# Kernel optimization log

Hardware: AMD Instinct MI355X
Metric: run time of the kernel (lower is better)

## Reference

```python
import jax, jax.numpy as jnp
import numpy as np

N = 100000
E = 1600000
D_IN = 128
HID = 128
OUT = 64


def _sage_conv(x, edge_index, W_l, W_r, b, num_nodes):
    # PyG SAGEConv (aggr='mean'): out = lin_l(mean_{j in N(i)} x_j) + lin_r(x_i)
    src, dst = edge_index[0], edge_index[1]
    msgs = x[src]  # [E, d] gather from source nodes
    summed = jax.ops.segment_sum(msgs, dst, num_segments=num_nodes)  # [N, d]
    cnt = jax.ops.segment_sum(jnp.ones((msgs.shape[0],), x.dtype), dst, num_segments=num_nodes)
    agg = summed / jnp.maximum(cnt, 1.0)[:, None]  # mean; isolated nodes -> 0
    return agg @ W_l + b + x @ W_r


def setup_inputs() -> dict:
    key = jax.random.key(0)
    ks = jax.random.split(key, 8)
    x = jax.random.normal(ks[0], (N, D_IN), dtype=jnp.float32)
    edge_index = jax.random.randint(ks[1], (2, E), 0, N, dtype=jnp.int64)
    s1 = 1.0 / np.sqrt(D_IN)
    s2 = 1.0 / np.sqrt(HID)
    W_l1 = jax.random.uniform(ks[2], (D_IN, HID), jnp.float32, -s1, s1)
    W_r1 = jax.random.uniform(ks[3], (D_IN, HID), jnp.float32, -s1, s1)
    b1 = jnp.zeros((HID,), jnp.float32)
    W_l2 = jax.random.uniform(ks[4], (HID, OUT), jnp.float32, -s2, s2)
    W_r2 = jax.random.uniform(ks[5], (HID, OUT), jnp.float32, -s2, s2)
    b2 = jnp.zeros((OUT,), jnp.float32)
    return {"x": x, "edge_index": edge_index, "W_l1": W_l1, "W_r1": W_r1,
            "b1": b1, "W_l2": W_l2, "W_r2": W_r2, "b2": b2}


def reference(x, edge_index, W_l1, W_r1, b1, W_l2, W_r2, b2):
    h = _sage_conv(x, edge_index, W_l1, W_r1, b1, N)
    h = jax.nn.relu(h)
    out = _sage_conv(h, edge_index, W_l2, W_r2, b2, N)
    return out
```

## Files before the change

kernel.cpp:

```cpp
#include <hip/hip_runtime.h>
#include <hip/hip_fp16.h>

typedef __attribute__((ext_vector_type(8))) short bf16x8;
typedef __attribute__((ext_vector_type(4))) float f32x4;

__device__ __forceinline__ f32x4 mfma16(bf16x8 a, bf16x8 b, f32x4 c) {
    return __builtin_amdgcn_mfma_f32_16x16x32_bf16(a, b, c, 0, 0, 0);
}

__device__ __forceinline__ unsigned short bf16_rte(float f) {
    unsigned int u = __float_as_uint(f);
    unsigned int r = (u + 0x7FFFu + ((u >> 16) & 1u)) >> 16;
    return (unsigned short)r;
}
__device__ __forceinline__ float bf16_f(unsigned short h) {
    return __uint_as_float(((unsigned int)h) << 16);
}

__global__ void k_wconv(const float* __restrict__ W, unsigned short* __restrict__ hi,
                        unsigned short* __restrict__ lo, int K, int F) {
    int e = blockIdx.x * 256 + threadIdx.x;
    if (e >= K * F) return;
    int col = e / K, k = e - col * K;
    float v = W[(size_t)k * F + col];
    unsigned short h = bf16_rte(v);
    hi[e] = h;
    lo[e] = bf16_rte(v - bf16_f(h));
}


#define MAXNB 1024

__global__ __launch_bounds__(256) void k_bcount(
    const int* __restrict__ dst, int* __restrict__ bcnt, int E, int chunk, int nb) {
    __shared__ int h[MAXNB];
    int t = threadIdx.x;
    for (int i = t; i < nb; i += 256) h[i] = 0;
    __syncthreads();
    int base = blockIdx.x * chunk;
    int end = min(base + chunk, E);
    for (int i = base + t; i < end; i += 256) atomicAdd(&h[dst[i] >> 7], 1);
    __syncthreads();
    for (int i = t; i < nb; i += 256)
        if (h[i]) atomicAdd(&bcnt[i], h[i]);
}

__global__ void k_bscan(const int* __restrict__ bcnt, int* __restrict__ boff,
                        int* __restrict__ bcur, int nb) {
    __shared__ int sh[1024];
    int t = threadIdx.x;
    int v = (t < nb) ? bcnt[t] : 0;
    sh[t] = v;
    __syncthreads();
    for (int off = 1; off < 1024; off <<= 1) {
        int u = (t >= off) ? sh[t - off] : 0;
        __syncthreads();
        sh[t] += u;
        __syncthreads();
    }
    if (t < nb) {
        int ex = sh[t] - v;
        boff[t] = ex;
        bcur[t] = ex;
    }
}

__global__ __launch_bounds__(256) void k_bscatter(
    const int* __restrict__ src, const int* __restrict__ dst,
    int* __restrict__ bcur, int2* __restrict__ pairs, int E, int chunk, int nb) {
    __shared__ int h[MAXNB];
    __shared__ int curs[MAXNB];
    int t = threadIdx.x;
    for (int i = t; i < nb; i += 256) h[i] = 0;
    __syncthreads();
    int base = blockIdx.x * chunk;
    int end = min(base + chunk, E);
    for (int i = base + t; i < end; i += 256) atomicAdd(&h[dst[i] >> 7], 1);
    __syncthreads();
    for (int i = t; i < nb; i += 256)
        curs[i] = h[i] ? atomicAdd(&bcur[i], h[i]) : 0;
    __syncthreads();
    for (int i = base + t; i < end; i += 256) {
        int d = dst[i];
        int p = atomicAdd(&curs[d >> 7], 1);
        pairs[p] = make_int2(d, src[i]);
    }
}

__global__ __launch_bounds__(256) void k_build(
    const int2* __restrict__ pairs, const int* __restrict__ boff,
    int* __restrict__ csr, int* __restrict__ start, int* __restrict__ deg,
    int n, int nb, int E) {
    __shared__ int scnt[128];
    __shared__ int soff[128];
    __shared__ int cur[128];
    int b = blockIdx.x;
    int t = threadIdx.x;
    int base = boff[b];
    int end = (b + 1 < nb) ? boff[b + 1] : E;
    if (t < 128) scnt[t] = 0;
    __syncthreads();
    for (int i = base + t; i < end; i += 256) {
        int2 e = pairs[i];
        atomicAdd(&scnt[e.x & 127], 1);
    }
    __syncthreads();
    if (t < 128) soff[t] = scnt[t];
    __syncthreads();
    for (int off = 1; off < 128; off <<= 1) {
        int val = 0;
        if (t < 128 && t >= off) val = soff[t - off];
        __syncthreads();
        if (t < 128) soff[t] += val;
        __syncthreads();
    }
    if (t < 128) {
        int c = scnt[t];
        int ex = soff[t] - c;
        int node = b * 128 + t;
        if (node < n) {
            start[node] = base + ex;
            deg[node] = c;
        }
        cur[t] = base + ex;
    }
    __syncthreads();
    for (int i = base + t; i < end; i += 256) {
        int2 e = pairs[i];
        int p = atomicAdd(&cur[e.x & 127], 1);
        csr[p] = e.y;
    }
}


#define SR 40

template <int FOUT>
__device__ __forceinline__ void gemm_fused_body(
    const float* __restrict__ X,
    const unsigned short* __restrict__ WHa, const unsigned short* __restrict__ WLa,
    const unsigned short* __restrict__ WHb, const unsigned short* __restrict__ WLb,
    const float* __restrict__ bias, __half* __restrict__ dstH,
    float* __restrict__ dstF, int n) {
    constexpr int CT = FOUT / 32;
    __shared__ unsigned short aHi[64 * SR], aLo[64 * SR];

    int t = threadIdx.x;
    int wv = t >> 6, l = t & 63, q = l >> 4, nl = l & 15;
    int ysel = wv >> 1;
    int wc = (wv & 1) * (FOUT / 2);
    int node0 = blockIdx.x * 64;
    const unsigned short* WH = ysel ? WHb : WHa;
    const unsigned short* WL = ysel ? WLb : WLa;

    int sn = t >> 2, q4 = t & 3;
    int gn = min(node0 + sn, n - 1);
    const float4* ap = (const float4*)(X + (size_t)gn * 128);

    f32x4 acc[4][CT];
#pragma unroll
    for (int a = 0; a < 4; ++a)
#pragma unroll
        for (int b = 0; b < CT; ++b) acc[a][b] = (f32x4){0.f, 0.f, 0.f, 0.f};

    float4 a0 = ap[q4 * 2];
    float4 a1 = ap[q4 * 2 + 1];

    bf16x8 wh[2][CT], wl[2][CT];
#pragma unroll
    for (int uu = 0; uu < CT; ++uu) {
        int base = (wc + uu * 16 + nl) * 128 + q * 8;
        wh[0][uu] = *(const bf16x8*)&WH[base];
        wl[0][uu] = *(const bf16x8*)&WL[base];
    }

    for (int c = 0; c < 4; ++c) {
        float4 n0, n1;
        if (c < 3) {
            n0 = ap[(c + 1) * 8 + q4 * 2];
            n1 = ap[(c + 1) * 8 + q4 * 2 + 1];
        }
        {
            int base = sn * SR + q4 * 8;
            ushort4 hi, lo;
            hi.x = bf16_rte(a0.x); lo.x = bf16_rte(a0.x - bf16_f(hi.x));
            hi.y = bf16_rte(a0.y); lo.y = bf16_rte(a0.y - bf16_f(hi.y));
            hi.z = bf16_rte(a0.z); lo.z = bf16_rte(a0.z - bf16_f(hi.z));
            hi.w = bf16_rte(a0.w); lo.w = bf16_rte(a0.w - bf16_f(hi.w));
            *(ushort4*)&aHi[base] = hi;
            *(ushort4*)&aLo[base] = lo;
            hi.x = bf16_rte(a1.x); lo.x = bf16_rte(a1.x - bf16_f(hi.x));
            hi.y = bf16_rte(a1.y); lo.y = bf16_rte(a1.y - bf16_f(hi.y));
            hi.z = bf16_rte(a1.z); lo.z = bf16_rte(a1.z - bf16_f(hi.z));
            hi.w = bf16_rte(a1.w); lo.w = bf16_rte(a1.w - bf16_f(hi.w));
            *(ushort4*)&aHi[base + 4] = hi;
            *(ushort4*)&aLo[base + 4] = lo;
        }
        __syncthreads();

        if (c < 3) {
#pragma unroll
            for (int uu = 0; uu < CT; ++uu) {
                int base = (wc + uu * 16 + nl) * 128 + (c + 1) * 32 + q * 8;
                wh[(c + 1) & 1][uu] = *(const bf16x8*)&WH[base];
                wl[(c + 1) & 1][uu] = *(const bf16x8*)&WL[base];
            }
        }

        bf16x8 ah[4], al[4];
#pragma unroll
        for (int tt = 0; tt < 4; ++tt) {
            int off = (tt * 16 + nl) * SR + q * 8;
            ah[tt] = *(const bf16x8*)&aHi[off];
            al[tt] = *(const bf16x8*)&aLo[off];
        }
        int cb = c & 1;
#pragma unroll
        for (int tt = 0; tt < 4; ++tt)
#pragma unroll
            for (int uu = 0; uu < CT; ++uu) {
                f32x4 a = acc[tt][uu];
                a = mfma16(al[tt], wh[cb][uu], a);
                a = mfma16(ah[tt], wl[cb][uu], a);
                a = mfma16(ah[tt], wh[cb][uu], a);
                acc[tt][uu] = a;
            }
        __syncthreads();
        if (c < 3) { a0 = n0; a1 = n1; }
    }

#pragma unroll
    for (int uu = 0; uu < CT; ++uu) {
        int col = wc + uu * 16 + nl;
        if (ysel) {
            float bv = bias[col];
#pragma unroll
            for (int tt = 0; tt < 4; ++tt)
#pragma unroll
                for (int r = 0; r < 4; ++r) {
                    int node = node0 + tt * 16 + q * 4 + r;
                    if (node < n) dstF[(size_t)node * FOUT + col] = acc[tt][uu][r] + bv;
                }
        } else {
#pragma unroll
            for (int tt = 0; tt < 4; ++tt)
#pragma unroll
                for (int r = 0; r < 4; ++r) {
                    int node = node0 + tt * 16 + q * 4 + r;
                    if (node < n) dstH[(size_t)node * FOUT + col] = __float2half(acc[tt][uu][r]);
                }
        }
    }
}

__global__ __launch_bounds__(256, 2) void gemm1(
    const float* __restrict__ X,
    const unsigned short* WHa, const unsigned short* WLa,
    const unsigned short* WHb, const unsigned short* WLb,
    const float* __restrict__ bias, __half* dstH, float* dstF, int n) {
    gemm_fused_body<128>(X, WHa, WLa, WHb, WLb, bias, dstH, dstF, n);
}

__global__ __launch_bounds__(256, 2) void gemm2(
    const float* __restrict__ X,
    const unsigned short* WHa, const unsigned short* WLa,
    const unsigned short* WHb, const unsigned short* WLb,
    const float* __restrict__ bias, __half* dstH, float* dstF, int n) {
    gemm_fused_body<64>(X, WHa, WLa, WHb, WLb, bias, dstH, dstF, n);
}


__global__ void agg1(const __half* __restrict__ u, const float* __restrict__ v,
                     const int* __restrict__ csr, const int* __restrict__ start,
                     const int* __restrict__ deg, float* __restrict__ h, int n) {
    int gid = blockIdx.x * blockDim.x + threadIdx.x;
    int wave = gid >> 6, lane = gid & 63;
    int half = lane >> 5, fl = lane & 31;
    int node = wave * 2 + half;
    if (node >= n) return;
    int s = start[node], d = deg[node];
    const float2* u2 = (const float2*)u;
    float4 A = {0.f, 0.f, 0.f, 0.f}, B = {0.f, 0.f, 0.f, 0.f};
    int j = 0;
    for (; j + 4 <= d; j += 4) {
        int i0 = csr[s + j], i1 = csr[s + j + 1], i2 = csr[s + j + 2], i3 = csr[s + j + 3];
        float2 r0 = u2[(size_t)i0 * 32 + fl];
        float2 r1 = u2[(size_t)i1 * 32 + fl];
        float2 r2 = u2[(size_t)i2 * 32 + fl];
        float2 r3 = u2[(size_t)i3 * 32 + fl];
        float2 a0 = __half22float2(*(const __half2*)&r0.x), b0 = __half22float2(*(const __half2*)&r0.y);
        float2 a1 = __half22float2(*(const __half2*)&r1.x), b1 = __half22float2(*(const __half2*)&r1.y);
        float2 a2 = __half22float2(*(const __half2*)&r2.x), b2 = __half22float2(*(const __half2*)&r2.y);
        float2 a3 = __half22float2(*(const __half2*)&r3.x), b3 = __half22float2(*(const __half2*)&r3.y);
        A.x += a0.x + a1.x; A.y += a0.y + a1.y;
        A.z += b0.x + b1.x; A.w += b0.y + b1.y;
        B.x += a2.x + a3.x; B.y += a2.y + a3.y;
        B.z += b2.x + b3.x; B.w += b2.y + b3.y;
    }
    for (; j < d; ++j) {
        float2 r0 = u2[(size_t)csr[s + j] * 32 + fl];
        float2 a0 = __half22float2(*(const __half2*)&r0.x), b0 = __half22float2(*(const __half2*)&r0.y);
        A.x += a0.x; A.y += a0.y; A.z += b0.x; A.w += b0.y;
    }
    float inv = 1.0f / (float)max(d, 1);
    float4 vv = ((const float4*)v)[(size_t)node * 32 + fl];
    float4 r;
    r.x = fmaxf((A.x + B.x) * inv + vv.x, 0.f);
    r.y = fmaxf((A.y + B.y) * inv + vv.y, 0.f);
    r.z = fmaxf((A.z + B.z) * inv + vv.z, 0.f);
    r.w = fmaxf((A.w + B.w) * inv + vv.w, 0.f);
    ((float4*)h)[(size_t)node * 32 + fl] = r;
}

__global__ void agg2(const __half* __restrict__ p, const int* __restrict__ csr,
                     const int* __restrict__ start, const int* __restrict__ deg,
                     float* __restrict__ out, int n) {
    int gid = blockIdx.x * blockDim.x + threadIdx.x;
    int wave = gid >> 6, lane = gid & 63;
    int half = lane >> 5, fl = lane & 31;
    int node = wave * 2 + half;
    if (node >= n) return;
    int s = start[node], d = deg[node];
    const __half2* p2 = (const __half2*)p;
    float ax = 0.f, ay = 0.f, bx = 0.f, by = 0.f, cx = 0.f, cy = 0.f, dx = 0.f, dy = 0.f;
    int j = 0;
    for (; j + 4 <= d; j += 4) {
        int i0 = csr[s + j], i1 = csr[s + j + 1], i2 = csr[s + j + 2], i3 = csr[s + j + 3];
        float2 v0 = __half22float2(p2[(size_t)i0 * 32 + fl]);
        float2 v1 = __half22float2(p2[(size_t)i1 * 32 + fl]);
        float2 v2 = __half22float2(p2[(size_t)i2 * 32 + fl]);
        float2 v3 = __half22float2(p2[(size_t)i3 * 32 + fl]);
        ax += v0.x; ay += v0.y;
        bx += v1.x; by += v1.y;
        cx += v2.x; cy += v2.y;
        dx += v3.x; dy += v3.y;
    }
    for (; j < d; ++j) {
        float2 v0 = __half22float2(p2[(size_t)csr[s + j] * 32 + fl]);
        ax += v0.x; ay += v0.y;
    }
    float inv = 1.0f / (float)max(d, 1);
    size_t o = (size_t)node * 32 + fl;
    float2 cu = ((float2*)out)[o];
    cu.x += ((ax + bx) + (cx + dx)) * inv;
    cu.y += ((ay + by) + (cy + dy)) * inv;
    ((float2*)out)[o] = cu;
}


extern "C" void kernel_launch(void* const* d_in, const int* in_sizes, int n_in,
                              void* d_out, int out_size, void* d_ws, size_t ws_size,
                              hipStream_t stream) {
    const float* x   = (const float*)d_in[0];
    const int*   ei  = (const int*)d_in[1];
    const float* Wl1 = (const float*)d_in[2];
    const float* Wr1 = (const float*)d_in[3];
    const float* b1  = (const float*)d_in[4];
    const float* Wl2 = (const float*)d_in[5];
    const float* Wr2 = (const float*)d_in[6];
    const float* b2  = (const float*)d_in[7];
    float* out = (float*)d_out;

    int Nn = in_sizes[0] / 128;
    int E  = in_sizes[1] / 2;
    const int* src = ei;
    const int* dst = ei + E;
    int nb = (Nn + 127) / 128;

    char* ws = (char*)d_ws;
    auto alloc = [&](size_t bytes) -> char* {
        char* pp = ws;
        ws += (bytes + 255) / 256 * 256;
        return pp;
    };
    int* bcnt   = (int*)alloc((size_t)nb * 4);
    int* boff   = (int*)alloc((size_t)nb * 4);
    int* bcur   = (int*)alloc((size_t)nb * 4);
    int* start  = (int*)alloc((size_t)Nn * 4);
    int* deg    = (int*)alloc((size_t)Nn * 4);
    int* csr    = (int*)alloc((size_t)E * 4);
    __half* u   = (__half*)alloc((size_t)Nn * 128 * 2);
    float* v    = (float*)alloc((size_t)Nn * 128 * 4);
    float* h    = (float*)alloc((size_t)Nn * 128 * 4);
    __half* p   = (__half*)alloc((size_t)Nn * 64 * 2);
    unsigned short* w1ah = (unsigned short*)alloc(128 * 128 * 2);
    unsigned short* w1al = (unsigned short*)alloc(128 * 128 * 2);
    unsigned short* w1bh = (unsigned short*)alloc(128 * 128 * 2);
    unsigned short* w1bl = (unsigned short*)alloc(128 * 128 * 2);
    unsigned short* w2ah = (unsigned short*)alloc(64 * 128 * 2);
    unsigned short* w2al = (unsigned short*)alloc(64 * 128 * 2);
    unsigned short* w2bh = (unsigned short*)alloc(64 * 128 * 2);
    unsigned short* w2bl = (unsigned short*)alloc(64 * 128 * 2);
    int2* pairs = (int2*)v;

    hipMemsetAsync(bcnt, 0, (size_t)nb * 4, stream);

    k_wconv<<<64, 256, 0, stream>>>(Wl1, w1ah, w1al, 128, 128);
    k_wconv<<<64, 256, 0, stream>>>(Wr1, w1bh, w1bl, 128, 128);
    k_wconv<<<32, 256, 0, stream>>>(Wl2, w2ah, w2al, 128, 64);
    k_wconv<<<32, 256, 0, stream>>>(Wr2, w2bh, w2bl, 128, 64);

    int chunk = (E + 255) / 256;
    k_bcount<<<256, 256, 0, stream>>>(dst, bcnt, E, chunk, nb);
    k_bscan<<<1, 1024, 0, stream>>>(bcnt, boff, bcur, nb);
    k_bscatter<<<256, 256, 0, stream>>>(src, dst, bcur, pairs, E, chunk, nb);
    k_build<<<nb, 256, 0, stream>>>(pairs, boff, csr, start, deg, Nn, nb, E);

    int gb = (Nn + 63) / 64;
    gemm1<<<gb, 256, 0, stream>>>(x, w1ah, w1al, w1bh, w1bl, b1, u, v, Nn);
    agg1<<<(Nn + 7) / 8, 256, 0, stream>>>(u, v, csr, start, deg, h, Nn);
    gemm2<<<gb, 256, 0, stream>>>(h, w2ah, w2al, w2bh, w2bl, b2, p, out, Nn);
    agg2<<<(Nn + 7) / 8, 256, 0, stream>>>(p, csr, start, deg, out, Nn);
}
```

Before: 382.7 us.

## Emit bf16 hi/lo split from agg1 and preload full A tile in GEMMs

agg1 now writes its ReLU output already split into bf16 hi and lo arrays, so gemm2 loads pre-split operands directly instead of converting fp32 inside the GEMM. Both GEMMs now stage all four K-chunks of the A tile into shared memory up front with a single barrier, replacing the per-chunk load/convert/sync loop. gemm2's launch bounds rise to 3 blocks per SM. Shared memory per block grows fourfold, which may limit occupancy, and the split conversion cost moves into agg1.

New measurement: 388.3 us. Within noise of the previous version (+1.4%).

```diff
diff --git a/kernel.cpp b/kernel.cpp
--- a/kernel.cpp
+++ b/kernel.cpp
@@ -135,15 +135,16 @@
 
 #define SR 40
 
-template <int FOUT>
+template <int FOUT, bool SPLIT>
 __device__ __forceinline__ void gemm_fused_body(
     const float* __restrict__ X,
+    const unsigned short* __restrict__ XH, const unsigned short* __restrict__ XL,
     const unsigned short* __restrict__ WHa, const unsigned short* __restrict__ WLa,
     const unsigned short* __restrict__ WHb, const unsigned short* __restrict__ WLb,
     const float* __restrict__ bias, __half* __restrict__ dstH,
     float* __restrict__ dstF, int n) {
     constexpr int CT = FOUT / 32;
-    __shared__ unsigned short aHi[64 * SR], aLo[64 * SR];
+    __shared__ unsigned short aHi[4][64 * SR], aLo[4][64 * SR];
 
     int t = threadIdx.x;
     int wv = t >> 6, l = t & 63, q = l >> 4, nl = l & 15;
@@ -155,16 +156,56 @@
 
     int sn = t >> 2, q4 = t & 3;
     int gn = min(node0 + sn, n - 1);
-    const float4* ap = (const float4*)(X + (size_t)gn * 128);
+
+    if (SPLIT) {
+        const unsigned short* xh0 = XH + (size_t)gn * 128 + q4 * 8;
+        const unsigned short* xl0 = XL + (size_t)gn * 128 + q4 * 8;
+        bf16x8 xh[4], xl[4];
+#pragma unroll
+        for (int c = 0; c < 4; ++c) {
+            xh[c] = *(const bf16x8*)(xh0 + c * 32);
+            xl[c] = *(const bf16x8*)(xl0 + c * 32);
+        }
+        int base = sn * SR + q4 * 8;
+#pragma unroll
+        for (int c = 0; c < 4; ++c) {
+            *(bf16x8*)&aHi[c][base] = xh[c];
+            *(bf16x8*)&aLo[c][base] = xl[c];
+        }
+    } else {
+        const float4* ap = (const float4*)(X + (size_t)gn * 128);
+        float4 xa[8];
+#pragma unroll
+        for (int c = 0; c < 4; ++c) {
+            xa[c * 2]     = ap[c * 8 + q4 * 2];
+            xa[c * 2 + 1] = ap[c * 8 + q4 * 2 + 1];
+        }
+        int base = sn * SR + q4 * 8;
+#pragma unroll
+        for (int c = 0; c < 4; ++c) {
+            ushort4 hi, lo;
+            float4 v = xa[c * 2];
+            hi.x = bf16_rte(v.x); lo.x = bf16_rte(v.x - bf16_f(hi.x));
+            hi.y = bf16_rte(v.y); lo.y = bf16_rte(v.y - bf16_f(hi.y));
+            hi.z = bf16_rte(v.z); lo.z = bf16_rte(v.z - bf16_f(hi.z));
+            hi.w = bf16_rte(v.w); lo.w = bf16_rte(v.w - bf16_f(hi.w));
+            *(ushort4*)&aHi[c][base] = hi;
+            *(ushort4*)&aLo[c][base] = lo;
+            v = xa[c * 2 + 1];
+            hi.x = bf16_rte(v.x); lo.x = bf16_rte(v.x - bf16_f(hi.x));
+            hi.y = bf16_rte(v.y); lo.y = bf16_rte(v.y - bf16_f(hi.y));
+            hi.z = bf16_rte(v.z); lo.z = bf16_rte(v.z - bf16_f(hi.z));
+            hi.w = bf16_rte(v.w); lo.w = bf16_rte(v.w - bf16_f(hi.w));
+            *(ushort4*)&aHi[c][base + 4] = hi;
+            *(ushort4*)&aLo[c][base + 4] = lo;
+        }
+    }
 
     f32x4 acc[4][CT];
 #pragma unroll
     for (int a = 0; a < 4; ++a)
 #pragma unroll
         for (int b = 0; b < CT; ++b) acc[a][b] = (f32x4){0.f, 0.f, 0.f, 0.f};
-
-    float4 a0 = ap[q4 * 2];
-    float4 a1 = ap[q4 * 2 + 1];
 
     bf16x8 wh[2][CT], wl[2][CT];
 #pragma unroll
@@ -174,30 +215,10 @@
         wl[0][uu] = *(const bf16x8*)&WL[base];
     }
 
+    __syncthreads();
+
+#pragma unroll
     for (int c = 0; c < 4; ++c) {
-        float4 n0, n1;
-        if (c < 3) {
-            n0 = ap[(c + 1) * 8 + q4 * 2];
-            n1 = ap[(c + 1) * 8 + q4 * 2 + 1];
-        }
-        {
-            int base = sn * SR + q4 * 8;
-            ushort4 hi, lo;
-            hi.x = bf16_rte(a0.x); lo.x = bf16_rte(a0.x - bf16_f(hi.x));
-            hi.y = bf16_rte(a0.y); lo.y = bf16_rte(a0.y - bf16_f(hi.y));
-            hi.z = bf16_rte(a0.z); lo.z = bf16_rte(a0.z - bf16_f(hi.z));
-            hi.w = bf16_rte(a0.w); lo.w = bf16_rte(a0.w - bf16_f(hi.w));
-            *(ushort4*)&aHi[base] = hi;
-            *(ushort4*)&aLo[base] = lo;
-            hi.x = bf16_rte(a1.x); lo.x = bf16_rte(a1.x - bf16_f(hi.x));
-            hi.y = bf16_rte(a1.y); lo.y = bf16_rte(a1.y - bf16_f(hi.y));
-            hi.z = bf16_rte(a1.z); lo.z = bf16_rte(a1.z - bf16_f(hi.z));
-            hi.w = bf16_rte(a1.w); lo.w = bf16_rte(a1.w - bf16_f(hi.w));
-            *(ushort4*)&aHi[base + 4] = hi;
-            *(ushort4*)&aLo[base + 4] = lo;
-        }
-        __syncthreads();
-
         if (c < 3) {
 #pragma unroll
             for (int uu = 0; uu < CT; ++uu) {
@@ -206,13 +227,12 @@
                 wl[(c + 1) & 1][uu] = *(const bf16x8*)&WL[base];
             }
         }
-
         bf16x8 ah[4], al[4];
 #pragma unroll
         for (int tt = 0; tt < 4; ++tt) {
             int off = (tt * 16 + nl) * SR + q * 8;
-            ah[tt] = *(const bf16x8*)&aHi[off];
-            al[tt] = *(const bf16x8*)&aLo[off];
+            ah[tt] = *(const bf16x8*)&aHi[c][off];
+            al[tt] = *(const bf16x8*)&aLo[c][off];
         }
         int cb = c & 1;
 #pragma unroll
@@ -225,8 +245,6 @@
                 a = mfma16(ah[tt], wh[cb][uu], a);
                 acc[tt][uu] = a;
             }
-        __syncthreads();
-        if (c < 3) { a0 = n0; a1 = n1; }
     }
 
 #pragma unroll
@@ -258,21 +276,22 @@
     const unsigned short* WHa, const unsigned short* WLa,
     const unsigned short* WHb, const unsigned short* WLb,
     const float* __restrict__ bias, __half* dstH, float* dstF, int n) {
-    gemm_fused_body<128>(X, WHa, WLa, WHb, WLb, bias, dstH, dstF, n);
-}
-
-__global__ __launch_bounds__(256, 2) void gemm2(
-    const float* __restrict__ X,
+    gemm_fused_body<128, false>(X, nullptr, nullptr, WHa, WLa, WHb, WLb, bias, dstH, dstF, n);
+}
+
+__global__ __launch_bounds__(256, 3) void gemm2(
+    const unsigned short* __restrict__ XH, const unsigned short* __restrict__ XL,
     const unsigned short* WHa, const unsigned short* WLa,
     const unsigned short* WHb, const unsigned short* WLb,
     const float* __restrict__ bias, __half* dstH, float* dstF, int n) {
-    gemm_fused_body<64>(X, WHa, WLa, WHb, WLb, bias, dstH, dstF, n);
+    gemm_fused_body<64, true>(nullptr, XH, XL, WHa, WLa, WHb, WLb, bias, dstH, dstF, n);
 }
 
 
 __global__ void agg1(const __half* __restrict__ u, const float* __restrict__ v,
                      const int* __restrict__ csr, const int* __restrict__ start,
-                     const int* __restrict__ deg, float* __restrict__ h, int n) {
+                     const int* __restrict__ deg, unsigned short* __restrict__ hHi,
+                     unsigned short* __restrict__ hLo, int n) {
     int gid = blockIdx.x * blockDim.x + threadIdx.x;
     int wave = gid >> 6, lane = gid & 63;
     int half = lane >> 5, fl = lane & 31;
@@ -309,7 +328,14 @@
     r.y = fmaxf((A.y + B.y) * inv + vv.y, 0.f);
     r.z = fmaxf((A.z + B.z) * inv + vv.z, 0.f);
     r.w = fmaxf((A.w + B.w) * inv + vv.w, 0.f);
-    ((float4*)h)[(size_t)node * 32 + fl] = r;
+    ushort4 hi, lo;
+    hi.x = bf16_rte(r.x); lo.x = bf16_rte(r.x - bf16_f(hi.x));
+    hi.y = bf16_rte(r.y); lo.y = bf16_rte(r.y - bf16_f(hi.y));
+    hi.z = bf16_rte(r.z); lo.z = bf16_rte(r.z - bf16_f(hi.z));
+    hi.w = bf16_rte(r.w); lo.w = bf16_rte(r.w - bf16_f(hi.w));
+    size_t ob = (size_t)node * 128 + fl * 4;
+    *(ushort4*)&hHi[ob] = hi;
+    *(ushort4*)&hLo[ob] = lo;
 }
 
 __global__ void agg2(const __half* __restrict__ p, const int* __restrict__ csr,
@@ -381,7 +407,8 @@
     int* csr    = (int*)alloc((size_t)E * 4);
     __half* u   = (__half*)alloc((size_t)Nn * 128 * 2);
     float* v    = (float*)alloc((size_t)Nn * 128 * 4);
-    float* h    = (float*)alloc((size_t)Nn * 128 * 4);
+    unsigned short* hHi = (unsigned short*)alloc((size_t)Nn * 128 * 4);
+    unsigned short* hLo = hHi + (size_t)Nn * 128;
     __half* p   = (__half*)alloc((size_t)Nn * 64 * 2);
     unsigned short* w1ah = (unsigned short*)alloc(128 * 128 * 2);
     unsigned short* w1al = (unsigned short*)alloc(128 * 128 * 2);
@@ -408,7 +435,7 @@
 
     int gb = (Nn + 63) / 64;
     gemm1<<<gb, 256, 0, stream>>>(x, w1ah, w1al, w1bh, w1bl, b1, u, v, Nn);
-    agg1<<<(Nn + 7) / 8, 256, 0, stream>>>(u, v, csr, start, deg, h, Nn);
-    gemm2<<<gb, 256, 0, stream>>>(h, w2ah, w2al, w2bh, w2bl, b2, p, out, Nn);
+    agg1<<<(Nn + 7) / 8, 256, 0, stream>>>(u, v, csr, start, deg, hHi, hLo, Nn);
+    gemm2<<<gb, 256, 0, stream>>>(hHi, hLo, w2ah, w2al, w2bh, w2bl, b2, p, out, Nn);
     agg2<<<(Nn + 7) / 8, 256, 0, stream>>>(p, csr, start, deg, out, Nn);
 }
```
